# Optimization experiments

Hardware: AMD Instinct MI355X
Metric: run time of the kernel (lower is better)

Reference implementation:

```python
import jax, jax.numpy as jnp
import numpy as np

N = 50000
E = 500000
F_IN = 128
H = 128
HEADS = 3
C = 10
G = 64
EPS = 1e-5
NEG_SLOPE = 0.2


def setup_inputs() -> dict:
    key = jax.random.key(0)
    ks = jax.random.split(key, 20)
    s = 0.1
    inp = {
        "x": jax.random.normal(ks[0], (N, F_IN), dtype=jnp.float32),
        "edge_index": jax.random.randint(ks[1], (2, E), 0, N, dtype=jnp.int64),
        "batch": jnp.sort(jax.random.randint(ks[2], (N,), 0, G, dtype=jnp.int64)),
        # GCNConv: lin weight + bias
        "W1": jax.random.normal(ks[3], (F_IN, H), dtype=jnp.float32) * s,
        "b1": jax.random.normal(ks[4], (H,), dtype=jnp.float32) * s,
        "gamma1": jnp.ones((H,), jnp.float32),
        "beta1": jnp.zeros((H,), jnp.float32),
        # SAGEConv: lin_l (neighbors, with bias) + lin_r (root, no bias)
        "Wl": jax.random.normal(ks[5], (H, H), dtype=jnp.float32) * s,
        "bl": jax.random.normal(ks[6], (H,), dtype=jnp.float32) * s,
        "Wr": jax.random.normal(ks[7], (H, H), dtype=jnp.float32) * s,
        "gamma2": jnp.ones((H,), jnp.float32),
        "beta2": jnp.zeros((H,), jnp.float32),
        # GATConv(heads=3, concat=False): lin + attention vectors + bias
        "W3": jax.random.normal(ks[8], (H, HEADS * H), dtype=jnp.float32) * s,
        "att_src": jax.random.normal(ks[9], (HEADS, H), dtype=jnp.float32) * s,
        "att_dst": jax.random.normal(ks[10], (HEADS, H), dtype=jnp.float32) * s,
        "b3": jax.random.normal(ks[11], (H,), dtype=jnp.float32) * s,
        "gamma3": jnp.ones((H,), jnp.float32),
        "beta3": jnp.zeros((H,), jnp.float32),
        # classifier
        "Wc": jax.random.normal(ks[12], (H, C), dtype=jnp.float32) * s,
        "bc": jax.random.normal(ks[13], (C,), dtype=jnp.float32) * s,
    }
    return inp


def _add_self_loops(src, dst):
    loop = jnp.arange(N, dtype=src.dtype)
    return jnp.concatenate([src, loop]), jnp.concatenate([dst, loop])


def _batch_norm(h, gamma, beta):
    mu = h.mean(axis=0)
    var = ((h - mu) ** 2).mean(axis=0)  # biased var, as torch BN training
    return (h - mu) * jax.lax.rsqrt(var + EPS) * gamma + beta


def gcn_conv(x, src, dst, W, b):
    s2, d2 = _add_self_loops(src, dst)
    deg = jax.ops.segment_sum(jnp.ones_like(d2, dtype=x.dtype), d2, num_segments=N)
    dinv = jnp.where(deg > 0, jax.lax.rsqrt(deg), 0.0)
    h = x @ W  # [N, H]
    norm = dinv[s2] * dinv[d2]  # [E+N]
    out = jax.ops.segment_sum(h[s2] * norm[:, None], d2, num_segments=N)
    return out + b


def sage_conv(x, src, dst, Wl, bl, Wr):
    # mean aggregation of neighbors + root transform
    deg = jax.ops.segment_sum(jnp.ones_like(dst, dtype=x.dtype), dst, num_segments=N)
    agg = jax.ops.segment_sum(x[src], dst, num_segments=N) / jnp.maximum(deg, 1.0)[:, None]
    return agg @ Wl + bl + x @ Wr


def gat_conv(x, src, dst, W, att_src, att_dst, b):
    s2, d2 = _add_self_loops(src, dst)
    h = (x @ W).reshape(N, HEADS, H)  # [N, heads, H]
    a_src = (h * att_src).sum(-1)  # [N, heads]
    a_dst = (h * att_dst).sum(-1)
    e = jax.nn.leaky_relu(a_src[s2] + a_dst[d2], NEG_SLOPE)  # [E2, heads]
    m = jax.ops.segment_max(e, d2, num_segments=N)  # stable softmax per target
    ex = jnp.exp(e - m[d2])
    denom = jax.ops.segment_sum(ex, d2, num_segments=N)
    alpha = ex / denom[d2]  # self-loops guarantee denom > 0
    out = jax.ops.segment_sum(h[s2] * alpha[:, :, None], d2, num_segments=N)
    return out.mean(axis=1) + b  # concat=False -> mean over heads


def reference(x, edge_index, batch, W1, b1, gamma1, beta1, Wl, bl, Wr,
              gamma2, beta2, W3, att_src, att_dst, b3, gamma3, beta3, Wc, bc):
    src, dst = edge_index[0], edge_index[1]
    h = jax.nn.elu(_batch_norm(gcn_conv(x, src, dst, W1, b1), gamma1, beta1))
    h = jax.nn.elu(_batch_norm(sage_conv(h, src, dst, Wl, bl, Wr), gamma2, beta2))
    h = jax.nn.elu(_batch_norm(gat_conv(h, src, dst, W3, att_src, att_dst, b3), gamma3, beta3))
    # global mean pool over graphs
    cnt = jax.ops.segment_sum(jnp.ones((N,), h.dtype), batch, num_segments=G)
    pooled = jax.ops.segment_sum(h, batch, num_segments=G) / jnp.maximum(cnt, 1.0)[:, None]
    logits = pooled @ Wc + bc
    return pooled, logits
```

## Files before the change

### kernel.cpp

```cpp
#include <hip/hip_runtime.h>
#include <math.h>

#define NN 50000
#define EE 500000
#define HH 128
#define NHEADS 3
#define CC 10
#define GG 64
#define EPSV 1e-5f
#define SLOPE 0.2f

typedef __attribute__((ext_vector_type(8))) short short8;
typedef __attribute__((ext_vector_type(4))) float f32x4;


__device__ __forceinline__ unsigned short f2b(float x) {
    unsigned int u = __builtin_bit_cast(unsigned int, x);
    return (unsigned short)((u + 0x7fffu + ((u >> 16) & 1u)) >> 16);
}
__device__ __forceinline__ unsigned int pack2(float a, float b) {
    return (unsigned int)f2b(a) | ((unsigned int)f2b(b) << 16);
}
__device__ __forceinline__ float2 b2f2(unsigned int u) {
    float2 r;
    r.x = __builtin_bit_cast(float, u << 16);
    r.y = __builtin_bit_cast(float, u & 0xffff0000u);
    return r;
}


__global__ void k_zero(int* __restrict__ deg, float* __restrict__ bn_sums,
                       float* __restrict__ poolacc) {
    int i = blockIdx.x * 256 + threadIdx.x;
    if (i < NN) deg[i] = 0;
    if (i < 768) bn_sums[i] = 0.f;
    if (i < GG * 128 + GG) poolacc[i] = 0.f;
}


__global__ void k_count_deg(const int* __restrict__ ei, int* __restrict__ deg) {
    int e = blockIdx.x * 256 + threadIdx.x;
    if (e < EE) atomicAdd(&deg[ei[EE + e]], 1);
}

__global__ void k_scan1(const int* __restrict__ deg, int* __restrict__ row_start,
                        int* __restrict__ blk) {
    __shared__ int s[256];
    int i = blockIdx.x * 256 + threadIdx.x;
    int v = (i < NN) ? deg[i] : 0;
    s[threadIdx.x] = v;
    __syncthreads();
    for (int o = 1; o < 256; o <<= 1) {
        int t = (threadIdx.x >= o) ? s[threadIdx.x - o] : 0;
        __syncthreads();
        s[threadIdx.x] += t;
        __syncthreads();
    }
    if (i < NN) row_start[i] = s[threadIdx.x] - v;
    if (threadIdx.x == 255) blk[blockIdx.x] = s[255];
}

__global__ void k_scan2(int* __restrict__ blk, int nb) {
    __shared__ int s[256];
    int v = (threadIdx.x < nb) ? blk[threadIdx.x] : 0;
    s[threadIdx.x] = v;
    __syncthreads();
    for (int o = 1; o < 256; o <<= 1) {
        int t = (threadIdx.x >= o) ? s[threadIdx.x - o] : 0;
        __syncthreads();
        s[threadIdx.x] += t;
        __syncthreads();
    }
    if (threadIdx.x < nb) blk[threadIdx.x] = s[threadIdx.x] - v;
}

__global__ void k_scan3(int* __restrict__ row_start, const int* __restrict__ blk,
                        const int* __restrict__ deg, int* __restrict__ cursor,
                        float* __restrict__ dinv, float* __restrict__ inv_sage) {
    int i = blockIdx.x * 256 + threadIdx.x;
    if (i < NN) {
        int rs = row_start[i] + blk[blockIdx.x];
        row_start[i] = rs;
        cursor[i] = rs;
        int d = deg[i];
        dinv[i] = rsqrtf((float)(d + 1));
        inv_sage[i] = 1.0f / (float)(d > 1 ? d : 1);
    }
}

__global__ void k_fill(const int* __restrict__ ei, int* __restrict__ cursor,
                       int* __restrict__ csr_src) {
    int e = blockIdx.x * 256 + threadIdx.x;
    if (e < EE) {
        int d = ei[EE + e];
        int p = atomicAdd(&cursor[d], 1);
        csr_src[p] = ei[e];
    }
}


__device__ __forceinline__ void split_store(float x, size_t dst, short* hi, short* lo) {
    unsigned int ux = __builtin_bit_cast(unsigned int, x);
    unsigned short hx = (unsigned short)(ux >> 16);
    float fx = __builtin_bit_cast(float, ux & 0xffff0000u);
    unsigned short lx = (unsigned short)(__builtin_bit_cast(unsigned int, x - fx) >> 16);
    hi[dst] = (short)hx;
    lo[dst] = (short)lx;
}

__device__ __forceinline__ void prep_one(float x, int k, int n, int cBase,
                                         short* hi, short* lo) {
    int c = (k >> 6) + cBase;
    int s = (k >> 5) & 1, quad = (k >> 3) & 3, j = k & 7;
    int G = n >> 4, l = quad * 16 + (n & 15);
    size_t dst = ((((size_t)(c * 2 + s)) * 8 + G) * 64 + l) * 8 + j;
    split_store(x, dst, hi, lo);
}

__global__ void k_prep_all(const float* __restrict__ W1, const float* __restrict__ Wl,
                           const float* __restrict__ Wr, const float* __restrict__ W3,
                           const float* __restrict__ att_src, const float* __restrict__ att_dst,
                           short* __restrict__ w1hi, short* __restrict__ w1lo,
                           short* __restrict__ wshi, short* __restrict__ wslo,
                           short* __restrict__ w3hi, short* __restrict__ w3lo,
                           float* __restrict__ wsrc, float* __restrict__ wdst) {
    int b = blockIdx.x, tid = threadIdx.x;
    if (b < 64) {
        int i = b * 256 + tid;
        prep_one(W1[i], i >> 7, i & 127, 0, w1hi, w1lo);
    } else if (b < 128) {
        int i = (b - 64) * 256 + tid;
        prep_one(Wl[i], i >> 7, i & 127, 0, wshi, wslo);
    } else if (b < 192) {
        int i = (b - 128) * 256 + tid;
        prep_one(Wr[i], i >> 7, i & 127, 2, wshi, wslo);
    } else if (b < 384) {
        int i = (b - 192) * 256 + tid;
        int k = i >> 7, n = i & 127;
        int h = k >> 7, kk = k & 127;
        float x = W3[(size_t)kk * 384 + h * 128 + n] * (1.f / 3.f);
        prep_one(x, k, n, 0, w3hi, w3lo);
    } else {
        for (int e = tid; e < 384; e += 256) {
            int h = e >> 7, k = e & 127;
            float s1 = 0.f, s2 = 0.f;
            const float* wrow = W3 + (size_t)k * 384 + h * 128;
            const float* as = att_src + h * 128;
            const float* ad = att_dst + h * 128;
            for (int j = 0; j < 128; j++) {
                float wv = wrow[j];
                s1 += wv * as[j];
                s2 += wv * ad[j];
            }
            wsrc[e] = s1;
            wdst[e] = s2;
        }
    }
}


template <bool ABF16, bool OUTB, bool STATS>
__global__ __launch_bounds__(256) void k_gemm_mfma(
    const void* __restrict__ A1v, const void* __restrict__ A2v,
    const short* __restrict__ Bhi, const short* __restrict__ Blo,
    const float* __restrict__ bias, void* __restrict__ Cv,
    float* __restrict__ sums, int M, int kc1, int kcT, int strideA1) {
    __shared__ short Ahi[128 * 72];
    __shared__ short Alo[ABF16 ? 8 : 128 * 72];
    __shared__ float cs[256];
    int tid = threadIdx.x;
    int rBase = blockIdx.x * 128;
    int wv = tid >> 6, lane = tid & 63;
    int rowHalf = wv >> 1, colHalf = wv & 1;
    int quad = lane >> 4, l15 = lane & 15;

    f32x4 acc[4][4];
#pragma unroll
    for (int a = 0; a < 4; a++)
#pragma unroll
        for (int b = 0; b < 4; b++) acc[a][b] = (f32x4)(0.f);

    for (int c = 0; c < kcT; c++) {
        const void* Asrc;
        int kOff, strideA;
        if (c < kc1) { Asrc = A1v; kOff = c * 64; strideA = strideA1; }
        else { Asrc = A2v; kOff = (c - kc1) * 64; strideA = 128; }

        __syncthreads();
        if (ABF16) {
            const unsigned short* As = (const unsigned short*)Asrc;
#pragma unroll
            for (int q = 0; q < 4; q++) {
                int slot = q * 256 + tid;
                int r = slot >> 3, k8 = slot & 7;
                uint4 v = make_uint4(0, 0, 0, 0);
                int gr = rBase + r;
                if (gr < M) v = *(const uint4*)(As + (size_t)gr * strideA + kOff + k8 * 8);
                *(uint4*)(Ahi + r * 72 + k8 * 8) = v;
            }
        } else {
            const float* As = (const float*)Asrc;
#pragma unroll
            for (int q8 = 0; q8 < 8; q8++) {
                int slot = q8 * 256 + tid;
                int r = slot >> 4, k4 = slot & 15;
                float4 v = make_float4(0.f, 0.f, 0.f, 0.f);
                int gr = rBase + r;
                if (gr < M) v = *(const float4*)(As + (size_t)gr * strideA + kOff + k4 * 4);
                unsigned int ux = __builtin_bit_cast(unsigned int, v.x);
                unsigned int uy = __builtin_bit_cast(unsigned int, v.y);
                unsigned int uz = __builtin_bit_cast(unsigned int, v.z);
                unsigned int uw = __builtin_bit_cast(unsigned int, v.w);
                unsigned int hx = ux >> 16, hy = uy >> 16, hz = uz >> 16, hw = uw >> 16;
                float fx = __builtin_bit_cast(float, ux & 0xffff0000u);
                float fy = __builtin_bit_cast(float, uy & 0xffff0000u);
                float fz = __builtin_bit_cast(float, uz & 0xffff0000u);
                float fw = __builtin_bit_cast(float, uw & 0xffff0000u);
                unsigned int lx = __builtin_bit_cast(unsigned int, v.x - fx) >> 16;
                unsigned int ly = __builtin_bit_cast(unsigned int, v.y - fy) >> 16;
                unsigned int lz = __builtin_bit_cast(unsigned int, v.z - fz) >> 16;
                unsigned int lw = __builtin_bit_cast(unsigned int, v.w - fw) >> 16;
                uint2 ph = make_uint2(hx | (hy << 16), hz | (hw << 16));
                uint2 pl = make_uint2(lx | (ly << 16), lz | (lw << 16));
                *(uint2*)(Ahi + r * 72 + k4 * 4) = ph;
                *(uint2*)(Alo + r * 72 + k4 * 4) = pl;
            }
        }
        __syncthreads();

#pragma unroll
        for (int s = 0; s < 2; s++) {
            short8 ah[4], al[4];
#pragma unroll
            for (int rb = 0; rb < 4; rb++) {
                int m = rowHalf * 64 + rb * 16 + l15;
                ah[rb] = *(const short8*)(Ahi + m * 72 + s * 32 + quad * 8);
                if (!ABF16) al[rb] = *(const short8*)(Alo + m * 72 + s * 32 + quad * 8);
            }
#pragma unroll
            for (int cg = 0; cg < 4; cg++) {
                int G = colHalf * 4 + cg;
                size_t bo = ((((size_t)(c * 2 + s)) * 8 + G) * 64 + lane) * 8;
                short8 bh = *(const short8*)(Bhi + bo);
                short8 bl = *(const short8*)(Blo + bo);
#pragma unroll
                for (int rb = 0; rb < 4; rb++) {
                    acc[rb][cg] = __builtin_amdgcn_mfma_f32_16x16x32_bf16(ah[rb], bh, acc[rb][cg], 0, 0, 0);
                    if (!ABF16)
                        acc[rb][cg] = __builtin_amdgcn_mfma_f32_16x16x32_bf16(al[rb], bh, acc[rb][cg], 0, 0, 0);
                    acc[rb][cg] = __builtin_amdgcn_mfma_f32_16x16x32_bf16(ah[rb], bl, acc[rb][cg], 0, 0, 0);
                }
            }
        }
    }

    if (STATS) {
        cs[tid] = 0.f;
        __syncthreads();
    }

#pragma unroll
    for (int cg = 0; cg < 4; cg++) {
        int col = colHalf * 64 + cg * 16 + l15;
        float bv = bias ? bias[col] : 0.f;
        float ps = 0.f, pq = 0.f;
#pragma unroll
        for (int rb = 0; rb < 4; rb++) {
#pragma unroll
            for (int r = 0; r < 4; r++) {
                int row = rBase + rowHalf * 64 + rb * 16 + quad * 4 + r;
                if (row < M) {
                    float ov = acc[rb][cg][r] + bv;
                    if (OUTB) ((unsigned short*)Cv)[(size_t)row * HH + col] = f2b(ov);
                    else ((float*)Cv)[(size_t)row * HH + col] = ov;
                    if (STATS) { ps += ov; pq += ov * ov; }
                }
            }
        }
        if (STATS) {
            ps += __shfl_xor(ps, 16, 64); ps += __shfl_xor(ps, 32, 64);
            pq += __shfl_xor(pq, 16, 64); pq += __shfl_xor(pq, 32, 64);
            if (quad == 0) {
                atomicAdd(&cs[col], ps);
                atomicAdd(&cs[128 + col], pq);
            }
        }
    }
    if (STATS) {
        __syncthreads();
        atomicAdd(&sums[tid], cs[tid]);
    }
}


__global__ void k_gcn_agg(const unsigned int* __restrict__ hb, const int* __restrict__ row_start,
                          const int* __restrict__ deg, const int* __restrict__ csr,
                          const float* __restrict__ dinv, const float* __restrict__ b1,
                          float* __restrict__ out, float* __restrict__ sums) {
    __shared__ float ls[256];
    int tid = threadIdx.x;
    int wv = tid >> 6, lane = tid & 63;
    float2 bb = ((const float2*)b1)[lane];
    float2 sacc = make_float2(0.f, 0.f), qacc = make_float2(0.f, 0.f);
    int nBase = (blockIdx.x * 4 + wv) * 8;
    for (int k = 0; k < 8; k++) {
        int n = nBase + k;
        if (n >= NN) break;
        float di = dinv[n];
        float2 hv = b2f2(hb[(size_t)n * 64 + lane]);
        float wsq = di * di;
        float2 acc = make_float2(hv.x * wsq, hv.y * wsq);
        int s0 = row_start[n], cnt = deg[n];
        int i = 0;
        for (; i + 4 <= cnt; i += 4) {
            int ss[4]; float ww[4]; unsigned int vv[4];
#pragma unroll
            for (int j = 0; j < 4; j++) ss[j] = csr[s0 + i + j];
#pragma unroll
            for (int j = 0; j < 4; j++) { ww[j] = dinv[ss[j]]; vv[j] = hb[(size_t)ss[j] * 64 + lane]; }
#pragma unroll
            for (int j = 0; j < 4; j++) {
                float2 v = b2f2(vv[j]);
                float wj = ww[j] * di;
                acc.x += v.x * wj; acc.y += v.y * wj;
            }
        }
        for (; i < cnt; i++) {
            int s = csr[s0 + i];
            float wj = dinv[s] * di;
            float2 v = b2f2(hb[(size_t)s * 64 + lane]);
            acc.x += v.x * wj; acc.y += v.y * wj;
        }
        acc.x += bb.x; acc.y += bb.y;
        ((float2*)out)[(size_t)n * 64 + lane] = acc;
        sacc.x += acc.x; sacc.y += acc.y;
        qacc.x += acc.x * acc.x; qacc.y += acc.y * acc.y;
    }
    ls[tid] = 0.f;
    __syncthreads();
    atomicAdd(&ls[2 * lane], sacc.x);
    atomicAdd(&ls[2 * lane + 1], sacc.y);
    atomicAdd(&ls[128 + 2 * lane], qacc.x);
    atomicAdd(&ls[128 + 2 * lane + 1], qacc.y);
    __syncthreads();
    atomicAdd(&sums[tid], ls[tid]);
}


__global__ void k_sage_agg(const unsigned int* __restrict__ hb, const int* __restrict__ row_start,
                           const int* __restrict__ deg, const int* __restrict__ csr,
                           const float* __restrict__ inv_sage, unsigned int* __restrict__ outb) {
    int n = blockIdx.x * 4 + (threadIdx.x >> 6);
    if (n >= NN) return;
    int lane = threadIdx.x & 63;
    float2 acc = make_float2(0.f, 0.f);
    int s0 = row_start[n], cnt = deg[n];
    int i = 0;
    for (; i + 4 <= cnt; i += 4) {
        int ss[4]; unsigned int vv[4];
#pragma unroll
        for (int j = 0; j < 4; j++) ss[j] = csr[s0 + i + j];
#pragma unroll
        for (int j = 0; j < 4; j++) vv[j] = hb[(size_t)ss[j] * 64 + lane];
#pragma unroll
        for (int j = 0; j < 4; j++) {
            float2 v = b2f2(vv[j]);
            acc.x += v.x; acc.y += v.y;
        }
    }
    for (; i < cnt; i++) {
        float2 v = b2f2(hb[(size_t)csr[s0 + i] * 64 + lane]);
        acc.x += v.x; acc.y += v.y;
    }
    float sc = inv_sage[n];
    outb[(size_t)n * 64 + lane] = pack2(acc.x * sc, acc.y * sc);
}


__device__ __forceinline__ float lrelu(float a) { return fmaxf(a, SLOPE * a); }

__global__ void k_gat_fused(const unsigned int* __restrict__ hb, const int* __restrict__ row_start,
                            const int* __restrict__ deg, const int* __restrict__ csr,
                            const float4* __restrict__ asrc4, const float4* __restrict__ adst4,
                            float4* __restrict__ alphaE, unsigned int* __restrict__ aggb) {
    int n = blockIdx.x * 4 + (threadIdx.x >> 6);
    if (n >= NN) return;
    int lane = threadIdx.x & 63;
    float4 ad = adst4[n], asv = asrc4[n];
    float es0 = lrelu(asv.x + ad.x), es1 = lrelu(asv.y + ad.y), es2 = lrelu(asv.z + ad.z);
    int s0 = row_start[n], cnt = deg[n];
    float self0, self1, self2;
    float al0 = 0.f, al1 = 0.f, al2 = 0.f;
    int sReg = 0;
    bool fast = (cnt <= 64);
    if (fast) {
        bool valid = lane < cnt;
        float e0 = -3e38f, e1 = -3e38f, e2 = -3e38f;
        if (valid) {
            sReg = csr[s0 + lane];
            float4 a4 = asrc4[sReg];
            e0 = lrelu(a4.x + ad.x); e1 = lrelu(a4.y + ad.y); e2 = lrelu(a4.z + ad.z);
        }
        float M0 = e0, M1 = e1, M2 = e2;
#pragma unroll
        for (int o = 32; o > 0; o >>= 1) {
            M0 = fmaxf(M0, __shfl_xor(M0, o, 64));
            M1 = fmaxf(M1, __shfl_xor(M1, o, 64));
            M2 = fmaxf(M2, __shfl_xor(M2, o, 64));
        }
        float m0 = fmaxf(es0, M0), m1 = fmaxf(es1, M1), m2 = fmaxf(es2, M2);
        float w0 = valid ? __expf(e0 - m0) : 0.f;
        float w1 = valid ? __expf(e1 - m1) : 0.f;
        float w2 = valid ? __expf(e2 - m2) : 0.f;
        float S0 = w0, S1 = w1, S2 = w2;
#pragma unroll
        for (int o = 32; o > 0; o >>= 1) {
            S0 += __shfl_xor(S0, o, 64);
            S1 += __shfl_xor(S1, o, 64);
            S2 += __shfl_xor(S2, o, 64);
        }
        float sw0 = __expf(es0 - m0), sw1 = __expf(es1 - m1), sw2 = __expf(es2 - m2);
        float r0 = 1.f / (S0 + sw0), r1 = 1.f / (S1 + sw1), r2 = 1.f / (S2 + sw2);
        al0 = w0 * r0; al1 = w1 * r1; al2 = w2 * r2;
        self0 = sw0 * r0; self1 = sw1 * r1; self2 = sw2 * r2;
    } else {
        float m0 = es0, m1 = es1, m2 = es2;
        for (int base = 0; base < cnt; base += 64) {
            int i2 = base + lane;
            float e0 = -3e38f, e1 = -3e38f, e2 = -3e38f;
            if (i2 < cnt) {
                int s = csr[s0 + i2];
                float4 a4 = asrc4[s];
                e0 = lrelu(a4.x + ad.x); e1 = lrelu(a4.y + ad.y); e2 = lrelu(a4.z + ad.z);
                alphaE[s0 + i2] = make_float4(e0, e1, e2, 0.f);
            }
#pragma unroll
            for (int o = 32; o > 0; o >>= 1) {
                e0 = fmaxf(e0, __shfl_xor(e0, o, 64));
                e1 = fmaxf(e1, __shfl_xor(e1, o, 64));
                e2 = fmaxf(e2, __shfl_xor(e2, o, 64));
            }
            m0 = fmaxf(m0, e0); m1 = fmaxf(m1, e1); m2 = fmaxf(m2, e2);
        }
        float l0 = __expf(es0 - m0), l1 = __expf(es1 - m1), l2 = __expf(es2 - m2);
        for (int base = 0; base < cnt; base += 64) {
            int i2 = base + lane;
            float w0 = 0.f, w1 = 0.f, w2 = 0.f;
            if (i2 < cnt) {
                float4 e = alphaE[s0 + i2];
                w0 = __expf(e.x - m0); w1 = __expf(e.y - m1); w2 = __expf(e.z - m2);
            }
#pragma unroll
            for (int o = 32; o > 0; o >>= 1) {
                w0 += __shfl_xor(w0, o, 64);
                w1 += __shfl_xor(w1, o, 64);
                w2 += __shfl_xor(w2, o, 64);
            }
            l0 += w0; l1 += w1; l2 += w2;
        }
        float r0 = 1.f / l0, r1 = 1.f / l1, r2 = 1.f / l2;
        self0 = __expf(es0 - m0) * r0;
        self1 = __expf(es1 - m1) * r1;
        self2 = __expf(es2 - m2) * r2;
        for (int base = 0; base < cnt; base += 64) {
            int i2 = base + lane;
            if (i2 < cnt) {
                float4 e = alphaE[s0 + i2];
                alphaE[s0 + i2] = make_float4(__expf(e.x - m0) * r0, __expf(e.y - m1) * r1,
                                              __expf(e.z - m2) * r2, 0.f);
            }
        }
    }

    float2 hv = b2f2(hb[(size_t)n * 64 + lane]);
    float2 a0 = make_float2(hv.x * self0, hv.y * self0);
    float2 a1 = make_float2(hv.x * self1, hv.y * self1);
    float2 a2 = make_float2(hv.x * self2, hv.y * self2);
    if (fast) {
        int i = 0;
        for (; i + 4 <= cnt; i += 4) {
            int ss[4]; unsigned int vv[4]; float aa0[4], aa1[4], aa2[4];
#pragma unroll
            for (int j = 0; j < 4; j++) {
                ss[j] = __shfl(sReg, i + j, 64);
                aa0[j] = __shfl(al0, i + j, 64);
                aa1[j] = __shfl(al1, i + j, 64);
                aa2[j] = __shfl(al2, i + j, 64);
            }
#pragma unroll
            for (int j = 0; j < 4; j++) vv[j] = hb[(size_t)ss[j] * 64 + lane];
#pragma unroll
            for (int j = 0; j < 4; j++) {
                float2 v = b2f2(vv[j]);
                a0.x += aa0[j] * v.x; a0.y += aa0[j] * v.y;
                a1.x += aa1[j] * v.x; a1.y += aa1[j] * v.y;
                a2.x += aa2[j] * v.x; a2.y += aa2[j] * v.y;
            }
        }
        for (; i < cnt; i++) {
            int s = __shfl(sReg, i, 64);
            float w0 = __shfl(al0, i, 64), w1 = __shfl(al1, i, 64), w2 = __shfl(al2, i, 64);
            float2 v = b2f2(hb[(size_t)s * 64 + lane]);
            a0.x += w0 * v.x; a0.y += w0 * v.y;
            a1.x += w1 * v.x; a1.y += w1 * v.y;
            a2.x += w2 * v.x; a2.y += w2 * v.y;
        }
    } else {
        for (int i = 0; i < cnt; i++) {
            int s = csr[s0 + i];
            float4 al = alphaE[s0 + i];
            float2 v = b2f2(hb[(size_t)s * 64 + lane]);
            a0.x += al.x * v.x; a0.y += al.x * v.y;
            a1.x += al.y * v.x; a1.y += al.y * v.y;
            a2.x += al.z * v.x; a2.y += al.z * v.y;
        }
    }
    unsigned int* op = aggb + (size_t)n * 192;
    op[lane] = pack2(a0.x, a0.y);
    op[64 + lane] = pack2(a1.x, a1.y);
    op[128 + lane] = pack2(a2.x, a2.y);
}


__device__ __forceinline__ float elu1(float x) { return x > 0.f ? x : (__expf(x) - 1.f); }

__device__ __forceinline__ float4 bn_apply4(float4 v, const float* sums,
                                            const float* gamma, const float* beta, int f4) {
    const float invN = 1.0f / NN;
    float4 s4 = *(const float4*)(sums + f4);
    float4 q4 = *(const float4*)(sums + 128 + f4);
    float4 g4 = *(const float4*)(gamma + f4);
    float4 b4 = *(const float4*)(beta + f4);
    float mx = s4.x * invN, my = s4.y * invN, mz = s4.z * invN, mw = s4.w * invN;
    float scx = rsqrtf(q4.x * invN - mx * mx + EPSV) * g4.x;
    float scy = rsqrtf(q4.y * invN - my * my + EPSV) * g4.y;
    float scz = rsqrtf(q4.z * invN - mz * mz + EPSV) * g4.z;
    float scw = rsqrtf(q4.w * invN - mw * mw + EPSV) * g4.w;
    v.x = elu1(v.x * scx + (b4.x - mx * scx));
    v.y = elu1(v.y * scy + (b4.y - my * scy));
    v.z = elu1(v.z * scz + (b4.z - mz * scz));
    v.w = elu1(v.w * scw + (b4.w - mw * scw));
    return v;
}

__global__ void k_bn_elu(const float* __restrict__ h, const float* __restrict__ sums,
                         const float* __restrict__ gamma, const float* __restrict__ beta,
                         unsigned int* __restrict__ hb) {
    int i = blockIdx.x * 256 + threadIdx.x;
    int f4 = (i & 31) << 2;
    float4 v = bn_apply4(((const float4*)h)[i], sums, gamma, beta, f4);
    uint2 p = make_uint2(pack2(v.x, v.y), pack2(v.z, v.w));
    *(uint2*)(hb + ((size_t)(i >> 5)) * 64 + (i & 31) * 2) = p;
}

__global__ void k_bn_elu_att(const float* __restrict__ h, const float* __restrict__ sums,
                             const float* __restrict__ gamma, const float* __restrict__ beta,
                             const float* __restrict__ wsrc, const float* __restrict__ wdst,
                             unsigned int* __restrict__ hb, float4* __restrict__ asrc4,
                             float4* __restrict__ adst4) {
    int i = blockIdx.x * 256 + threadIdx.x;
    int fi = i & 31;
    int f4 = fi << 2;
    float4 v = bn_apply4(((const float4*)h)[i], sums, gamma, beta, f4);
    uint2 p = make_uint2(pack2(v.x, v.y), pack2(v.z, v.w));
    *(uint2*)(hb + ((size_t)(i >> 5)) * 64 + fi * 2) = p;
    const float4* ws4 = (const float4*)wsrc;
    const float4* wd4 = (const float4*)wdst;
    float d[6];
#pragma unroll
    for (int hd = 0; hd < 3; hd++) {
        float4 a = ws4[hd * 32 + fi];
        float4 b = wd4[hd * 32 + fi];
        d[hd] = v.x * a.x + v.y * a.y + v.z * a.z + v.w * a.w;
        d[3 + hd] = v.x * b.x + v.y * b.y + v.z * b.z + v.w * b.w;
    }
#pragma unroll
    for (int o = 16; o > 0; o >>= 1) {
#pragma unroll
        for (int j = 0; j < 6; j++) d[j] += __shfl_xor(d[j], o, 64);
    }
    if ((threadIdx.x & 31) == 0) {
        int r = i >> 5;
        asrc4[r] = make_float4(d[0], d[1], d[2], 0.f);
        adst4[r] = make_float4(d[3], d[4], d[5], 0.f);
    }
}


#define POOL_BLOCKS 800

__global__ void k_pool_bn(const float* __restrict__ h, const int* __restrict__ batch,
                          const float* __restrict__ sums, const float* __restrict__ gamma,
                          const float* __restrict__ beta, float* __restrict__ pool,
                          float* __restrict__ cntf) {
    const int RP = (NN + POOL_BLOCKS - 1) / POOL_BLOCKS;
    int r0 = blockIdx.x * RP;
    int r1 = r0 + RP;
    if (r1 > NN) r1 = NN;
    if (r0 >= r1) return;
    int f = threadIdx.x;
    const float invN = 1.0f / NN;
    float mu = sums[f] * invN;
    float var = sums[128 + f] * invN - mu * mu;
    float sc = rsqrtf(var + EPSV) * gamma[f];
    float sh = beta[f] - mu * sc;
    int g = batch[r0];
    float s = 0.f, c = 0.f;
    for (int r = r0; r < r1; r++) {
        int gr = batch[r];
        if (gr != g) {
            atomicAdd(&pool[g * 128 + f], s);
            if (f == 0) atomicAdd(&cntf[g], c);
            s = 0.f; c = 0.f; g = gr;
        }
        s += elu1(h[(size_t)r * 128 + f] * sc + sh);
        c += 1.f;
    }
    atomicAdd(&pool[g * 128 + f], s);
    if (f == 0) atomicAdd(&cntf[g], c);
}

__global__ void k_pool_fin(const float* __restrict__ pool, const float* __restrict__ cntf,
                           const float* __restrict__ Wc, const float* __restrict__ bc,
                           float* __restrict__ outp) {
    __shared__ float pr[128];
    int g = blockIdx.x, f = threadIdx.x;
    float c = fmaxf(cntf[g], 1.f);
    float pv = pool[g * 128 + f] / c;
    outp[g * 128 + f] = pv;
    pr[f] = pv;
    __syncthreads();
    if (f < CC) {
        float s = bc[f];
        for (int k = 0; k < 128; k++) s += pr[k] * Wc[k * CC + f];
        outp[GG * HH + g * CC + f] = s;
    }
}


extern "C" void kernel_launch(void* const* d_in, const int* in_sizes, int n_in,
                              void* d_out, int out_size, void* d_ws, size_t ws_size,
                              hipStream_t stream) {
    const float* x = (const float*)d_in[0];
    const int* ei = (const int*)d_in[1];
    const int* batch = (const int*)d_in[2];
    const float* W1 = (const float*)d_in[3];
    const float* b1 = (const float*)d_in[4];
    const float* gamma1 = (const float*)d_in[5];
    const float* beta1 = (const float*)d_in[6];
    const float* Wl = (const float*)d_in[7];
    const float* bl = (const float*)d_in[8];
    const float* Wr = (const float*)d_in[9];
    const float* gamma2 = (const float*)d_in[10];
    const float* beta2 = (const float*)d_in[11];
    const float* W3 = (const float*)d_in[12];
    const float* att_src = (const float*)d_in[13];
    const float* att_dst = (const float*)d_in[14];
    const float* b3 = (const float*)d_in[15];
    const float* gamma3 = (const float*)d_in[16];
    const float* beta3 = (const float*)d_in[17];
    const float* Wc = (const float*)d_in[18];
    const float* bc = (const float*)d_in[19];

    char* w = (char*)d_ws;
    size_t o = 0;
    float* bufA = (float*)(w + o); o += (size_t)NN * 128 * 4;
    float* bufC = (float*)(w + o); o += (size_t)NN * 128 * 4;
    unsigned int* h0b = (unsigned int*)(w + o); o += (size_t)NN * 128 * 2;
    unsigned int* h1b = (unsigned int*)(w + o); o += (size_t)NN * 128 * 2;
    unsigned int* sageb = (unsigned int*)(w + o); o += (size_t)NN * 128 * 2;
    unsigned int* h2b = (unsigned int*)(w + o); o += (size_t)NN * 128 * 2;
    unsigned int* aggDb = (unsigned int*)(w + o); o += (size_t)NN * 384 * 2;
    int* csr = (int*)(w + o); o += (size_t)EE * 4;
    int* deg = (int*)(w + o); o += (size_t)NN * 4;
    int* row_start = (int*)(w + o); o += (size_t)NN * 4;
    int* cursor = (int*)(w + o); o += (size_t)NN * 4;
    float* dinv = (float*)(w + o); o += (size_t)NN * 4;
    float* inv_sage = (float*)(w + o); o += (size_t)NN * 4;
    float4* asrc4 = (float4*)(w + o); o += (size_t)NN * 16;
    float4* adst4 = (float4*)(w + o); o += (size_t)NN * 16;
    float* bn_sums = (float*)(w + o); o += 3 * 256 * 4;
    int* blk = (int*)(w + o); o += 1024;
    float* poolacc = (float*)(w + o); o += (size_t)GG * 128 * 4;
    float* cntf = (float*)(w + o); o += (size_t)GG * 4;
    float* wsrc = (float*)(w + o); o += 384 * 4;
    float* wdst = (float*)(w + o); o += 384 * 4;
    float4* alphaE = (float4*)(w + o); o += (size_t)EE * 16;
    short* w1hi = (short*)(w + o); o += (size_t)128 * 128 * 2;
    short* w1lo = (short*)(w + o); o += (size_t)128 * 128 * 2;
    short* wshi = (short*)(w + o); o += (size_t)256 * 128 * 2;
    short* wslo = (short*)(w + o); o += (size_t)256 * 128 * 2;
    short* w3hi = (short*)(w + o); o += (size_t)384 * 128 * 2;
    short* w3lo = (short*)(w + o); o += (size_t)384 * 128 * 2;

    float* outp = (float*)d_out;

    const int NB_SCAN = (NN + 255) / 256;
    const int EB = (EE + 255) / 256;
    const int NW4 = (NN + 3) / 4;
    const int NW32 = (NN + 31) / 32;
    const int GB = (NN + 127) / 128;

    k_zero<<<NB_SCAN, 256, 0, stream>>>(deg, bn_sums, poolacc);
    k_count_deg<<<EB, 256, 0, stream>>>(ei, deg);
    k_scan1<<<NB_SCAN, 256, 0, stream>>>(deg, row_start, blk);
    k_scan2<<<1, 256, 0, stream>>>(blk, NB_SCAN);
    k_scan3<<<NB_SCAN, 256, 0, stream>>>(row_start, blk, deg, cursor, dinv, inv_sage);
    k_fill<<<EB, 256, 0, stream>>>(ei, cursor, csr);
    k_prep_all<<<385, 256, 0, stream>>>(W1, Wl, Wr, W3, att_src, att_dst, w1hi, w1lo,
                                        wshi, wslo, w3hi, w3lo, wsrc, wdst);

    k_gemm_mfma<false, true, false><<<GB, 256, 0, stream>>>(x, nullptr, w1hi, w1lo, nullptr,
                                                            h0b, nullptr, NN, 2, 2, 128);
    k_gcn_agg<<<NW32, 256, 0, stream>>>(h0b, row_start, deg, csr, dinv, b1, bufA, bn_sums);
    k_bn_elu<<<NN * 32 / 256, 256, 0, stream>>>(bufA, bn_sums, gamma1, beta1, h1b);

    k_sage_agg<<<NW4, 256, 0, stream>>>(h1b, row_start, deg, csr, inv_sage, sageb);
    k_gemm_mfma<true, false, true><<<GB, 256, 0, stream>>>(sageb, h1b, wshi, wslo, bl, bufC,
                                                           bn_sums + 256, NN, 2, 4, 128);
    k_bn_elu_att<<<NN * 32 / 256, 256, 0, stream>>>(bufC, bn_sums + 256, gamma2, beta2,
                                                    wsrc, wdst, h2b, asrc4, adst4);

    k_gat_fused<<<NW4, 256, 0, stream>>>(h2b, row_start, deg, csr, asrc4, adst4, alphaE, aggDb);
    k_gemm_mfma<true, false, true><<<GB, 256, 0, stream>>>(aggDb, nullptr, w3hi, w3lo, b3, bufA,
                                                           bn_sums + 512, NN, 6, 6, 384);

    k_pool_bn<<<POOL_BLOCKS, 128, 0, stream>>>(bufA, batch, bn_sums + 512, gamma3, beta3,
                                               poolacc, cntf);
    k_pool_fin<<<GG, 128, 0, stream>>>(poolacc, cntf, Wc, bc, outp);
}
```

Before: 455.8 us.

## Store GCN and GAT pre-BN outputs in bf16 and replicate BN stat atomics

The GCN aggregation now handles one node per wave instead of eight and writes its pre-BatchNorm output as packed bf16 rather than fp32. Its BatchNorm partial sums go into 32 replicated accumulators, which a new single-block kernel then reduces. The GAT projection GEMM also writes bf16, so the pooling kernel reads half the bytes. This cuts global traffic for the large intermediates and spreads atomic contention on the stats, at the cost of an extra launch, more blocks and rounding of the pre-normalization values to bf16.

```diff
diff --git a/kernel.cpp b/kernel.cpp
--- a/kernel.cpp
+++ b/kernel.cpp
@@ -29,11 +29,12 @@
 }
 
 
-__global__ void k_zero(int* __restrict__ deg, float* __restrict__ bn_sums,
-                       float* __restrict__ poolacc) {
+__global__ void k_zero(int* __restrict__ deg, float* __restrict__ bn_rep,
+                       float* __restrict__ bn_sums23, float* __restrict__ poolacc) {
     int i = blockIdx.x * 256 + threadIdx.x;
     if (i < NN) deg[i] = 0;
-    if (i < 768) bn_sums[i] = 0.f;
+    if (i < 32 * 256) bn_rep[i] = 0.f;
+    if (i < 512) bn_sums23[i] = 0.f;
     if (i < GG * 128 + GG) poolacc[i] = 0.f;
 }
 
@@ -296,16 +297,13 @@
 __global__ void k_gcn_agg(const unsigned int* __restrict__ hb, const int* __restrict__ row_start,
                           const int* __restrict__ deg, const int* __restrict__ csr,
                           const float* __restrict__ dinv, const float* __restrict__ b1,
-                          float* __restrict__ out, float* __restrict__ sums) {
+                          unsigned int* __restrict__ outb, float* __restrict__ bn_rep) {
     __shared__ float ls[256];
     int tid = threadIdx.x;
     int wv = tid >> 6, lane = tid & 63;
-    float2 bb = ((const float2*)b1)[lane];
+    int n = blockIdx.x * 4 + wv;
     float2 sacc = make_float2(0.f, 0.f), qacc = make_float2(0.f, 0.f);
-    int nBase = (blockIdx.x * 4 + wv) * 8;
-    for (int k = 0; k < 8; k++) {
-        int n = nBase + k;
-        if (n >= NN) break;
+    if (n < NN) {
         float di = dinv[n];
         float2 hv = b2f2(hb[(size_t)n * 64 + lane]);
         float wsq = di * di;
@@ -331,10 +329,11 @@
             float2 v = b2f2(hb[(size_t)s * 64 + lane]);
             acc.x += v.x * wj; acc.y += v.y * wj;
         }
+        float2 bb = ((const float2*)b1)[lane];
         acc.x += bb.x; acc.y += bb.y;
-        ((float2*)out)[(size_t)n * 64 + lane] = acc;
-        sacc.x += acc.x; sacc.y += acc.y;
-        qacc.x += acc.x * acc.x; qacc.y += acc.y * acc.y;
+        outb[(size_t)n * 64 + lane] = pack2(acc.x, acc.y);
+        sacc = acc;
+        qacc = make_float2(acc.x * acc.x, acc.y * acc.y);
     }
     ls[tid] = 0.f;
     __syncthreads();
@@ -343,7 +342,14 @@
     atomicAdd(&ls[128 + 2 * lane], qacc.x);
     atomicAdd(&ls[128 + 2 * lane + 1], qacc.y);
     __syncthreads();
-    atomicAdd(&sums[tid], ls[tid]);
+    atomicAdd(&bn_rep[(blockIdx.x & 31) * 256 + tid], ls[tid]);
+}
+
+__global__ void k_bn_reduce(const float* __restrict__ rep, float* __restrict__ sums) {
+    int t = threadIdx.x;
+    float s = 0.f;
+    for (int r = 0; r < 32; r++) s += rep[r * 256 + t];
+    sums[t] = s;
 }
 
 
@@ -543,14 +549,17 @@
     return v;
 }
 
-__global__ void k_bn_elu(const float* __restrict__ h, const float* __restrict__ sums,
-                         const float* __restrict__ gamma, const float* __restrict__ beta,
-                         unsigned int* __restrict__ hb) {
+__global__ void k_bn_elu_b(const unsigned int* __restrict__ hpre, const float* __restrict__ sums,
+                           const float* __restrict__ gamma, const float* __restrict__ beta,
+                           unsigned int* __restrict__ hb) {
     int i = blockIdx.x * 256 + threadIdx.x;
     int f4 = (i & 31) << 2;
-    float4 v = bn_apply4(((const float4*)h)[i], sums, gamma, beta, f4);
-    uint2 p = make_uint2(pack2(v.x, v.y), pack2(v.z, v.w));
-    *(uint2*)(hb + ((size_t)(i >> 5)) * 64 + (i & 31) * 2) = p;
+    uint2 p = *(const uint2*)(hpre + (size_t)(i >> 5) * 64 + (i & 31) * 2);
+    float2 v01 = b2f2(p.x), v23 = b2f2(p.y);
+    float4 v = make_float4(v01.x, v01.y, v23.x, v23.y);
+    v = bn_apply4(v, sums, gamma, beta, f4);
+    uint2 q = make_uint2(pack2(v.x, v.y), pack2(v.z, v.w));
+    *(uint2*)(hb + (size_t)(i >> 5) * 64 + (i & 31) * 2) = q;
 }
 
 __global__ void k_bn_elu_att(const float* __restrict__ h, const float* __restrict__ sums,
@@ -589,7 +598,7 @@
 
 #define POOL_BLOCKS 800
 
-__global__ void k_pool_bn(const float* __restrict__ h, const int* __restrict__ batch,
+__global__ void k_pool_bn(const unsigned int* __restrict__ hb, const int* __restrict__ batch,
                           const float* __restrict__ sums, const float* __restrict__ gamma,
                           const float* __restrict__ beta, float* __restrict__ pool,
                           float* __restrict__ cntf) {
@@ -613,7 +622,10 @@
             if (f == 0) atomicAdd(&cntf[g], c);
             s = 0.f; c = 0.f; g = gr;
         }
-        s += elu1(h[(size_t)r * 128 + f] * sc + sh);
+        unsigned int u = hb[(size_t)r * 64 + (f >> 1)];
+        float2 vv = b2f2(u);
+        float hv = (f & 1) ? vv.y : vv.x;
+        s += elu1(hv * sc + sh);
         c += 1.f;
     }
     atomicAdd(&pool[g * 128 + f], s);
@@ -664,13 +676,14 @@
 
     char* w = (char*)d_ws;
     size_t o = 0;
-    float* bufA = (float*)(w + o); o += (size_t)NN * 128 * 4;
     float* bufC = (float*)(w + o); o += (size_t)NN * 128 * 4;
     unsigned int* h0b = (unsigned int*)(w + o); o += (size_t)NN * 128 * 2;
+    unsigned int* h1pre = (unsigned int*)(w + o); o += (size_t)NN * 128 * 2;
     unsigned int* h1b = (unsigned int*)(w + o); o += (size_t)NN * 128 * 2;
     unsigned int* sageb = (unsigned int*)(w + o); o += (size_t)NN * 128 * 2;
     unsigned int* h2b = (unsigned int*)(w + o); o += (size_t)NN * 128 * 2;
     unsigned int* aggDb = (unsigned int*)(w + o); o += (size_t)NN * 384 * 2;
+    unsigned int* h3b = (unsigned int*)(w + o); o += (size_t)NN * 128 * 2;
     int* csr = (int*)(w + o); o += (size_t)EE * 4;
     int* deg = (int*)(w + o); o += (size_t)NN * 4;
     int* row_start = (int*)(w + o); o += (size_t)NN * 4;
@@ -679,7 +692,9 @@
     float* inv_sage = (float*)(w + o); o += (size_t)NN * 4;
     float4* asrc4 = (float4*)(w + o); o += (size_t)NN * 16;
     float4* adst4 = (float4*)(w + o); o += (size_t)NN * 16;
-    float* bn_sums = (float*)(w + o); o += 3 * 256 * 4;
+    float* bn_rep = (float*)(w + o); o += 32 * 256 * 4;
+    float* bn1 = (float*)(w + o); o += 256 * 4;
+    float* bn_sums23 = (float*)(w + o); o += 512 * 4;
     int* blk = (int*)(w + o); o += 1024;
     float* poolacc = (float*)(w + o); o += (size_t)GG * 128 * 4;
     float* cntf = (float*)(w + o); o += (size_t)GG * 4;
@@ -698,10 +713,9 @@
     const int NB_SCAN = (NN + 255) / 256;
     const int EB = (EE + 255) / 256;
     const int NW4 = (NN + 3) / 4;
-    const int NW32 = (NN + 31) / 32;
     const int GB = (NN + 127) / 128;
 
-    k_zero<<<NB_SCAN, 256, 0, stream>>>(deg, bn_sums, poolacc);
+    k_zero<<<NB_SCAN, 256, 0, stream>>>(deg, bn_rep, bn_sums23, poolacc);
     k_count_deg<<<EB, 256, 0, stream>>>(ei, deg);
     k_scan1<<<NB_SCAN, 256, 0, stream>>>(deg, row_start, blk);
     k_scan2<<<1, 256, 0, stream>>>(blk, NB_SCAN);
@@ -712,20 +726,21 @@
 
     k_gemm_mfma<false, true, false><<<GB, 256, 0, stream>>>(x, nullptr, w1hi, w1lo, nullptr,
                                                             h0b, nullptr, NN, 2, 2, 128);
-    k_gcn_agg<<<NW32, 256, 0, stream>>>(h0b, row_start, deg, csr, dinv, b1, bufA, bn_sums);
-    k_bn_elu<<<NN * 32 / 256, 256, 0, stream>>>(bufA, bn_sums, gamma1, beta1, h1b);
+    k_gcn_agg<<<NW4, 256, 0, stream>>>(h0b, row_start, deg, csr, dinv, b1, h1pre, bn_rep);
+    k_bn_reduce<<<1, 256, 0, stream>>>(bn_rep, bn1);
+    k_bn_elu_b<<<NN * 32 / 256, 256, 0, stream>>>(h1pre, bn1, gamma1, beta1, h1b);
 
     k_sage_agg<<<NW4, 256, 0, stream>>>(h1b, row_start, deg, csr, inv_sage, sageb);
     k_gemm_mfma<true, false, true><<<GB, 256, 0, stream>>>(sageb, h1b, wshi, wslo, bl, bufC,
-                                                           bn_sums + 256, NN, 2, 4, 128);
-    k_bn_elu_att<<<NN * 32 / 256, 256, 0, stream>>>(bufC, bn_sums + 256, gamma2, beta2,
+                                                           bn_sums23, NN, 2, 4, 128);
+    k_bn_elu_att<<<NN * 32 / 256, 256, 0, stream>>>(bufC, bn_sums23, gamma2, beta2,
                                                     wsrc, wdst, h2b, asrc4, adst4);
 
     k_gat_fused<<<NW4, 256, 0, stream>>>(h2b, row_start, deg, csr, asrc4, adst4, alphaE, aggDb);
-    k_gemm_mfma<true, false, true><<<GB, 256, 0, stream>>>(aggDb, nullptr, w3hi, w3lo, b3, bufA,
-                                                           bn_sums + 512, NN, 6, 6, 384);
-
-    k_pool_bn<<<POOL_BLOCKS, 128, 0, stream>>>(bufA, batch, bn_sums + 512, gamma3, beta3,
+    k_gemm_mfma<true, true, true><<<GB, 256, 0, stream>>>(aggDb, nullptr, w3hi, w3lo, b3, h3b,
+                                                          bn_sums23 + 256, NN, 6, 6, 384);
+
+    k_pool_bn<<<POOL_BLOCKS, 128, 0, stream>>>(h3b, batch, bn_sums23 + 256, gamma3, beta3,
                                                poolacc, cntf);
     k_pool_fin<<<GG, 128, 0, stream>>>(poolacc, cntf, Wc, bc, outp);
 }
```

After: 463.8 us. No clear change (+1.8%).
